# Performance work log

Hardware: AMD Instinct MI355X
Metric: run time of the kernel (lower is better)

## Reference

```python
import jax, jax.numpy as jnp
import numpy as np

NEG_SLOPE = 0.2

def _gat(x_src, x_dst, W_src, W_dst, a_src, a_dst, bias, src, dst, num_dst):
    # Bipartite PyG GATConv, heads=1, concat, add_self_loops=False.
    h_src = x_src @ W_src              # [N_src, H]
    h_dst = x_dst @ W_dst              # [N_dst, H]
    # Per-edge attention logits: leaky_relu(a_src.h_src[i] + a_dst.h_dst[j])
    e = jax.nn.leaky_relu((h_src @ a_src)[src] + (h_dst @ a_dst)[dst], NEG_SLOPE)  # [E]
    # Segment softmax over incoming edges of each dst node
    m = jax.ops.segment_max(e, dst, num_segments=num_dst)
    m = jnp.where(jnp.isfinite(m), m, 0.0)  # empty segments -> safe
    ex = jnp.exp(e - m[dst])
    denom = jax.ops.segment_sum(ex, dst, num_segments=num_dst)
    alpha = ex / denom[dst]            # [E]
    # Scatter-sum weighted source messages
    out = jax.ops.segment_sum(alpha[:, None] * h_src[src], dst, num_segments=num_dst)
    return out + bias


def setup_inputs() -> dict:
    key = jax.random.key(0)
    ks = jax.random.split(key, 20)
    N_L, N_A, D, H, O, E = 100000, 20000, 128, 128, 64, 500000
    s = 1.0 / np.sqrt(D)
    inp = {
        'x_label': jax.random.normal(ks[0], (N_L, D), jnp.float32),
        'x_attr': jax.random.normal(ks[1], (N_A, D), jnp.float32),
        'W_src_la': jax.random.normal(ks[2], (D, H), jnp.float32) * s,
        'W_dst_la': jax.random.normal(ks[3], (D, H), jnp.float32) * s,
        'a_src_la': jax.random.normal(ks[4], (H,), jnp.float32) * s,
        'a_dst_la': jax.random.normal(ks[5], (H,), jnp.float32) * s,
        'b_la': jax.random.normal(ks[6], (H,), jnp.float32) * 0.01,
        'W_src_al': jax.random.normal(ks[7], (D, H), jnp.float32) * s,
        'W_dst_al': jax.random.normal(ks[8], (D, H), jnp.float32) * s,
        'a_src_al': jax.random.normal(ks[9], (H,), jnp.float32) * s,
        'a_dst_al': jax.random.normal(ks[10], (H,), jnp.float32) * s,
        'b_al': jax.random.normal(ks[11], (H,), jnp.float32) * 0.01,
        'W_lin': jax.random.normal(ks[12], (H, O), jnp.float32) * s,
        'b_lin': jax.random.normal(ks[13], (O,), jnp.float32) * 0.01,
        'edge_src_la': jax.random.randint(ks[14], (E,), 0, N_L, jnp.int32),
        'edge_dst_la': jax.random.randint(ks[15], (E,), 0, N_A, jnp.int32),
        'edge_src_al': jax.random.randint(ks[16], (E,), 0, N_A, jnp.int32),
        'edge_dst_al': jax.random.randint(ks[17], (E,), 0, N_L, jnp.int32),
    }
    return inp


def reference(x_label, x_attr, W_src_la, W_dst_la, a_src_la, a_dst_la, b_la,
              W_src_al, W_dst_al, a_src_al, a_dst_al, b_al, W_lin, b_lin,
              edge_src_la, edge_dst_la, edge_src_al, edge_dst_al):
    N_L = x_label.shape[0]
    N_A = x_attr.shape[0]
    # label -> attribute GAT (output for 'attribute' nodes)
    h_attr = _gat(x_label, x_attr, W_src_la, W_dst_la, a_src_la, a_dst_la, b_la,
                  edge_src_la, edge_dst_la, N_A)
    # attribute -> label GAT (output for 'label' nodes)
    h_label = _gat(x_attr, x_label, W_src_al, W_dst_al, a_src_al, a_dst_al, b_al,
                   edge_src_al, edge_dst_al, N_L)
    h_attr = jax.nn.relu(h_attr)  # computed as in original (unused downstream)
    h_label = jax.nn.relu(h_label)
    out = h_label @ W_lin + b_lin
    return out
```

## Files before the change

### kernel.cpp

```cpp
#include <hip/hip_runtime.h>
#include <math.h>

#define NEG_SLOPE 0.2f

typedef __attribute__((ext_vector_type(8))) short bf16x8;
typedef __attribute__((ext_vector_type(4))) float f32x4;

__device__ __forceinline__ unsigned short f2bf(float f) {
    unsigned u = __float_as_uint(f);
    unsigned r = (u + 0x7FFFu + ((u >> 16) & 1u)) >> 16;
    return (unsigned short)r;
}

__device__ __forceinline__ void acc8(float* a, uint4 u, float x) {
    a[0] += x * __uint_as_float(u.x << 16);
    a[1] += x * __uint_as_float(u.x & 0xFFFF0000u);
    a[2] += x * __uint_as_float(u.y << 16);
    a[3] += x * __uint_as_float(u.y & 0xFFFF0000u);
    a[4] += x * __uint_as_float(u.z << 16);
    a[5] += x * __uint_as_float(u.z & 0xFFFF0000u);
    a[6] += x * __uint_as_float(u.w << 16);
    a[7] += x * __uint_as_float(u.w & 0xFFFF0000u);
}

__device__ __forceinline__ unsigned pack2(unsigned short lo, unsigned short hi) {
    return (unsigned)lo | ((unsigned)hi << 16);
}

__global__ __launch_bounds__(256) void k_pre(
    const int* __restrict__ dst, int* __restrict__ deg, int E, int nbDeg,
    const float* __restrict__ Wd, const float* __restrict__ ad,
    const float* __restrict__ Ws, const float* __restrict__ as_,
    float* __restrict__ wdst, float* __restrict__ wsrc,
    const float* __restrict__ Wlin, unsigned short* __restrict__ Wb) {
    int b = blockIdx.x, t = threadIdx.x;
    if (b < nbDeg) {
        int i = b * 256 + t;
        if (i < E) atomicAdd(&deg[dst[i]], 1);
    } else if (b == nbDeg) {
        const float* W = (t < 128) ? Wd : Ws;
        const float* a = (t < 128) ? ad : as_;
        int d = t & 127;
        float s = 0.f;
        #pragma unroll 8
        for (int h = 0; h < 128; ++h) s += W[d * 128 + h] * a[h];
        if (t < 128) wdst[d] = s; else wsrc[d] = s;
    } else {
        int idx = (b - nbDeg - 1) * 256 + t;
        int col = idx >> 7, k = idx & 127;
        Wb[idx] = f2bf(Wlin[k * 64 + col]);
    }
}

__device__ __forceinline__ void rowdot_role(const float* __restrict__ X,
                                            const float* __restrict__ v,
                                            float* __restrict__ out, int n,
                                            int vb, int t) {
    int gw = vb * 4 + (t >> 6);
    int lane = t & 63;
    int half = lane >> 5, li = lane & 31;
    int row = gw * 2 + half;
    if (row >= n) return;
    const float4* X4 = (const float4*)X;
    const float4* V4 = (const float4*)v;
    float4 x = X4[(size_t)row * 32 + li];
    float4 b = V4[li];
    float p = x.x * b.x + x.y * b.y + x.z * b.z + x.w * b.w;
    #pragma unroll
    for (int off = 16; off; off >>= 1) p += __shfl_xor(p, off);
    if (li == 0) out[row] = p;
}

__device__ __forceinline__ void hsrc_role(const float* __restrict__ X,
                                          const float* __restrict__ W,
                                          unsigned short* __restrict__ Hb,
                                          int nrows, int row0, int t,
                                          float* __restrict__ Xs ) {
    #pragma unroll
    for (int i = 0; i < 16; ++i) {
        int idx = t + i * 256;
        int r = idx >> 7;
        Xs[r * 128 + (idx & 127)] = (row0 + r < nrows) ? X[(size_t)row0 * 128 + idx] : 0.f;
    }
    __syncthreads();
    int cg = t & 31, rg = t >> 5;
    float acc[4][4];
    #pragma unroll
    for (int i = 0; i < 4; ++i)
        #pragma unroll
        for (int j = 0; j < 4; ++j) acc[i][j] = 0.f;
    const float4* W4 = (const float4*)W;
    #pragma unroll 4
    for (int d = 0; d < 128; ++d) {
        float4 wv = W4[d * 32 + cg];
        float x0 = Xs[(rg * 4 + 0) * 128 + d], x1 = Xs[(rg * 4 + 1) * 128 + d];
        float x2 = Xs[(rg * 4 + 2) * 128 + d], x3 = Xs[(rg * 4 + 3) * 128 + d];
        acc[0][0] += x0 * wv.x; acc[0][1] += x0 * wv.y; acc[0][2] += x0 * wv.z; acc[0][3] += x0 * wv.w;
        acc[1][0] += x1 * wv.x; acc[1][1] += x1 * wv.y; acc[1][2] += x1 * wv.z; acc[1][3] += x1 * wv.w;
        acc[2][0] += x2 * wv.x; acc[2][1] += x2 * wv.y; acc[2][2] += x2 * wv.z; acc[2][3] += x2 * wv.w;
        acc[3][0] += x3 * wv.x; acc[3][1] += x3 * wv.y; acc[3][2] += x3 * wv.z; acc[3][3] += x3 * wv.w;
    }
    #pragma unroll
    for (int i = 0; i < 4; ++i) {
        int gr = row0 + rg * 4 + i;
        if (gr < nrows) {
            ushort4 o;
            o.x = f2bf(acc[i][0]); o.y = f2bf(acc[i][1]);
            o.z = f2bf(acc[i][2]); o.w = f2bf(acc[i][3]);
            *(ushort4*)&Hb[(size_t)gr * 128 + cg * 4] = o;
        }
    }
}

__global__ __launch_bounds__(256) void k_mid(
    const int* __restrict__ deg, int* __restrict__ bsum, int nScan, int n,
    const float* __restrict__ xL, const float* __restrict__ wdst,
    float* __restrict__ sdst, int nRL, int NL,
    const float* __restrict__ xA, const float* __restrict__ wsrc,
    float* __restrict__ ssrc, int nRA, int NA,
    const float* __restrict__ Wsrc, unsigned short* __restrict__ Hb) {
    __shared__ float smemf[32 * 128];
    int b = blockIdx.x, t = threadIdx.x;
    if (b < nScan) {
        int* sd = (int*)smemf;
        int base = b * 1024 + t * 4;
        int s = 0;
        #pragma unroll
        for (int i = 0; i < 4; ++i) if (base + i < n) s += deg[base + i];
        sd[t] = s;
        __syncthreads();
        for (int off = 128; off; off >>= 1) {
            if (t < off) sd[t] += sd[t + off];
            __syncthreads();
        }
        if (t == 0) bsum[b] = sd[0];
    } else if (b < nScan + nRL) {
        rowdot_role(xL, wdst, sdst, NL, b - nScan, t);
    } else if (b < nScan + nRL + nRA) {
        rowdot_role(xA, wsrc, ssrc, NA, b - nScan - nRL, t);
    } else {
        hsrc_role(xA, Wsrc, Hb, NA, (b - nScan - nRL - nRA) * 32, t, smemf);
    }
}

__global__ __launch_bounds__(128) void k_scanB(int* __restrict__ bsum, int nb,
                                               int* __restrict__ rowptr, int n, int E) {
    __shared__ int ss[128];
    int t = threadIdx.x;
    if (nb <= 128) {
        int v = (t < nb) ? bsum[t] : 0;
        ss[t] = v;
        __syncthreads();
        for (int off = 1; off < 128; off <<= 1) {
            int u = (t >= off) ? ss[t - off] : 0;
            __syncthreads();
            ss[t] += u;
            __syncthreads();
        }
        if (t < nb) bsum[t] = ss[t] - v;
    } else if (t == 0) {
        int run = 0;
        for (int i = 0; i < nb; ++i) { int v = bsum[i]; bsum[i] = run; run += v; }
    }
    if (t == 0) rowptr[n] = E;
}

__global__ __launch_bounds__(256) void k_scanC(const int* __restrict__ deg,
                                               const int* __restrict__ bsum,
                                               int* __restrict__ rowptr, int n) {
    __shared__ int ss[256];
    int t = threadIdx.x;
    int base = blockIdx.x * 1024 + t * 4;
    int d[4]; int tsum = 0;
    #pragma unroll
    for (int i = 0; i < 4; ++i) { d[i] = (base + i < n) ? deg[base + i] : 0; tsum += d[i]; }
    ss[t] = tsum;
    __syncthreads();
    for (int off = 1; off < 256; off <<= 1) {
        int v = (t >= off) ? ss[t - off] : 0;
        __syncthreads();
        ss[t] += v;
        __syncthreads();
    }
    int excl = ss[t] - tsum + bsum[blockIdx.x];
    #pragma unroll
    for (int i = 0; i < 4; ++i) {
        if (base + i < n) rowptr[base + i] = excl;
        excl += d[i];
    }
}

__global__ void k_scatter(const int* __restrict__ src, const int* __restrict__ dst,
                          const float* __restrict__ ssrc, const float* __restrict__ sdst,
                          const int* __restrict__ rowptr, int* __restrict__ cursor,
                          int2* __restrict__ csr_pair, int E) {
    int i = blockIdx.x * blockDim.x + threadIdx.x;
    if (i >= E) return;
    int s = src[i], d = dst[i];
    float e = ssrc[s] + sdst[d];
    e = e > 0.f ? e : NEG_SLOPE * e;
    float ex = __expf(e);
    int pos = rowptr[d] + atomicAdd(&cursor[d], 1);
    csr_pair[pos] = make_int2(s, __float_as_int(ex));
}

__global__ __launch_bounds__(256) void k_gatout(
    const int* __restrict__ rowptr, const int2* __restrict__ csr_pair,
    const unsigned short* __restrict__ Hb, const float* __restrict__ b_al,
    const unsigned short* __restrict__ Wb, const float* __restrict__ b_lin,
    float* __restrict__ out, int n) {
    __shared__ unsigned short Gs[64 * 128];
    int t = threadIdx.x;
    int wave = t >> 6, lane = t & 63;
    int grp = lane >> 4, gl = lane & 15;
    const uint4* H16 = (const uint4*)Hb;
    int row0b = blockIdx.x * 64;
    const float4* B4 = (const float4*)b_al;
    float4 bA = B4[gl * 2], bB = B4[gl * 2 + 1];

    #pragma unroll
    for (int rr = 0; rr < 4; ++rr) {
        int rl = wave * 16 + rr * 4 + grp;
        int row = row0b + rl;
        uint4 gpack = make_uint4(0u, 0u, 0u, 0u);
        if (row < n) {
            int beg = rowptr[row], end = rowptr[row + 1];
            float a[8];
            #pragma unroll
            for (int k = 0; k < 8; ++k) a[k] = 0.f;
            float denom = 0.f;
            int j = beg;
            for (; j + 4 <= end; j += 4) {
                int2 p0 = csr_pair[j], p1 = csr_pair[j + 1];
                int2 p2 = csr_pair[j + 2], p3 = csr_pair[j + 3];
                float x0 = __int_as_float(p0.y), x1 = __int_as_float(p1.y);
                float x2 = __int_as_float(p2.y), x3 = __int_as_float(p3.y);
                uint4 u0 = H16[(size_t)p0.x * 16 + gl];
                uint4 u1 = H16[(size_t)p1.x * 16 + gl];
                uint4 u2 = H16[(size_t)p2.x * 16 + gl];
                uint4 u3 = H16[(size_t)p3.x * 16 + gl];
                denom += (x0 + x1) + (x2 + x3);
                acc8(a, u0, x0); acc8(a, u1, x1); acc8(a, u2, x2); acc8(a, u3, x3);
            }
            for (; j + 2 <= end; j += 2) {
                int2 p0 = csr_pair[j], p1 = csr_pair[j + 1];
                float x0 = __int_as_float(p0.y), x1 = __int_as_float(p1.y);
                uint4 u0 = H16[(size_t)p0.x * 16 + gl];
                uint4 u1 = H16[(size_t)p1.x * 16 + gl];
                denom += x0 + x1;
                acc8(a, u0, x0); acc8(a, u1, x1);
            }
            if (j < end) {
                int2 p0 = csr_pair[j];
                float x0 = __int_as_float(p0.y);
                uint4 u0 = H16[(size_t)p0.x * 16 + gl];
                denom += x0;
                acc8(a, u0, x0);
            }
            float inv = denom > 0.f ? 1.f / denom : 0.f;
            unsigned short g0 = f2bf(fmaxf(a[0] * inv + bA.x, 0.f));
            unsigned short g1 = f2bf(fmaxf(a[1] * inv + bA.y, 0.f));
            unsigned short g2 = f2bf(fmaxf(a[2] * inv + bA.z, 0.f));
            unsigned short g3 = f2bf(fmaxf(a[3] * inv + bA.w, 0.f));
            unsigned short g4 = f2bf(fmaxf(a[4] * inv + bB.x, 0.f));
            unsigned short g5 = f2bf(fmaxf(a[5] * inv + bB.y, 0.f));
            unsigned short g6 = f2bf(fmaxf(a[6] * inv + bB.z, 0.f));
            unsigned short g7 = f2bf(fmaxf(a[7] * inv + bB.w, 0.f));
            gpack = make_uint4(pack2(g0, g1), pack2(g2, g3), pack2(g4, g5), pack2(g6, g7));
        }
        int slot = gl ^ (rl & 15);
        *(uint4*)&Gs[rl * 128 + slot * 8] = gpack;
    }
    __syncthreads();

    int m = lane & 15, kq = lane >> 4;
    int rl = wave * 16 + m;
    f32x4 acc0 = {0.f, 0.f, 0.f, 0.f};
    f32x4 acc1 = {0.f, 0.f, 0.f, 0.f};
    f32x4 acc2 = {0.f, 0.f, 0.f, 0.f};
    f32x4 acc3 = {0.f, 0.f, 0.f, 0.f};
    const bf16x8* B0 = (const bf16x8*)(Wb + (size_t)(0 * 16 + m) * 128);
    const bf16x8* B1 = (const bf16x8*)(Wb + (size_t)(1 * 16 + m) * 128);
    const bf16x8* B2 = (const bf16x8*)(Wb + (size_t)(2 * 16 + m) * 128);
    const bf16x8* B3 = (const bf16x8*)(Wb + (size_t)(3 * 16 + m) * 128);
    #pragma unroll
    for (int s = 0; s < 4; ++s) {
        int ci = s * 4 + kq;
        int slot = ci ^ m;
        bf16x8 a = *(const bf16x8*)&Gs[rl * 128 + slot * 8];
        acc0 = __builtin_amdgcn_mfma_f32_16x16x32_bf16(a, B0[ci], acc0, 0, 0, 0);
        acc1 = __builtin_amdgcn_mfma_f32_16x16x32_bf16(a, B1[ci], acc1, 0, 0, 0);
        acc2 = __builtin_amdgcn_mfma_f32_16x16x32_bf16(a, B2[ci], acc2, 0, 0, 0);
        acc3 = __builtin_amdgcn_mfma_f32_16x16x32_bf16(a, B3[ci], acc3, 0, 0, 0);
    }
    float bl0 = b_lin[0 * 16 + m], bl1 = b_lin[1 * 16 + m];
    float bl2 = b_lin[2 * 16 + m], bl3 = b_lin[3 * 16 + m];
    int row0 = row0b + wave * 16;
    #pragma unroll
    for (int j = 0; j < 4; ++j) {
        int row = row0 + kq * 4 + j;
        if (row < n) {
            float* orow = out + (size_t)row * 64;
            orow[0 * 16 + m] = acc0[j] + bl0;
            orow[1 * 16 + m] = acc1[j] + bl1;
            orow[2 * 16 + m] = acc2[j] + bl2;
            orow[3 * 16 + m] = acc3[j] + bl3;
        }
    }
}

extern "C" void kernel_launch(void* const* d_in, const int* in_sizes, int n_in,
                              void* d_out, int out_size, void* d_ws, size_t ws_size,
                              hipStream_t stream) {
    const float* x_label  = (const float*)d_in[0];
    const float* x_attr   = (const float*)d_in[1];
    const float* W_src_al = (const float*)d_in[7];
    const float* W_dst_al = (const float*)d_in[8];
    const float* a_src_al = (const float*)d_in[9];
    const float* a_dst_al = (const float*)d_in[10];
    const float* b_al     = (const float*)d_in[11];
    const float* W_lin    = (const float*)d_in[12];
    const float* b_lin    = (const float*)d_in[13];
    const int* edge_src   = (const int*)d_in[16];
    const int* edge_dst   = (const int*)d_in[17];

    const int D = 128;
    const int N_L = in_sizes[0] / D;
    const int N_A = in_sizes[1] / D;
    const int E   = in_sizes[16];

    const int nbDeg = (E + 255) / 256;
    const int nScan = (N_L + 1023) / 1024;
    const int nRL   = (N_L + 7) / 8;
    const int nRA   = (N_A + 7) / 8;
    const int nH    = (N_A + 31) / 32;

    float* ws = (float*)d_ws;
    float* s_src = ws;
    float* s_dst = s_src + N_A;
    float* wdst  = s_dst + N_L;
    float* wsrc  = wdst + 128;
    int*   deg    = (int*)(wsrc + 128);
    int*   cursor = deg + N_L;
    int*   bsum   = cursor + N_L;
    int*   rowptr = bsum + 128;
    int2*  csr_pair = (int2*)(rowptr + N_L + 4);
    unsigned short* Hb = (unsigned short*)(csr_pair + E);
    unsigned short* Wb = Hb + (size_t)N_A * 128;

    float* out = (float*)d_out;

    hipMemsetAsync(deg, 0, (size_t)2 * N_L * sizeof(int), stream);

    k_pre<<<nbDeg + 1 + 32, 256, 0, stream>>>(edge_dst, deg, E, nbDeg,
                                              W_dst_al, a_dst_al, W_src_al, a_src_al,
                                              wdst, wsrc, W_lin, Wb);
    k_mid<<<nScan + nRL + nRA + nH, 256, 0, stream>>>(
        deg, bsum, nScan, N_L,
        x_label, wdst, s_dst, nRL, N_L,
        x_attr, wsrc, s_src, nRA, N_A,
        W_src_al, Hb);
    k_scanB<<<1, 128, 0, stream>>>(bsum, nScan, rowptr, N_L, E);
    k_scanC<<<nScan, 256, 0, stream>>>(deg, bsum, rowptr, N_L);
    k_scatter<<<nbDeg, 256, 0, stream>>>(edge_src, edge_dst, s_src, s_dst,
                                         rowptr, cursor, csr_pair, E);
    k_gatout<<<(N_L + 63) / 64, 256, 0, stream>>>(rowptr, csr_pair, Hb, b_al,
                                                  Wb, b_lin, out, N_L);
}
```

Measured before the change: 257.5 us.

## Fold prefix-scan into k_mid and batch more rows per rowdot wave

Replaces the three-pass scan (block sums in k_mid, k_scanB, k_scanC) with a single scan role inside k_mid. Each scan block recomputes its prefix offset by summing all preceding degrees with int4 loads, then does its local scan. This removes two kernel launches and the serial dependency between them. The rowdot role now handles 4 rows per half-wave, cutting block count for the dot products, and the block order is changed so the GEMM blocks launch first. The cost is redundant prefix reads, which grow with block index, and extra registers per thread.

```diff
diff --git a/kernel.cpp b/kernel.cpp
--- a/kernel.cpp
+++ b/kernel.cpp
@@ -56,19 +56,34 @@
                                             const float* __restrict__ v,
                                             float* __restrict__ out, int n,
                                             int vb, int t) {
-    int gw = vb * 4 + (t >> 6);
-    int lane = t & 63;
+    int wave = t >> 6, lane = t & 63;
     int half = lane >> 5, li = lane & 31;
-    int row = gw * 2 + half;
-    if (row >= n) return;
+    int row0 = (vb * 4 + wave) * 8 + half;
     const float4* X4 = (const float4*)X;
     const float4* V4 = (const float4*)v;
-    float4 x = X4[(size_t)row * 32 + li];
-    float4 b = V4[li];
-    float p = x.x * b.x + x.y * b.y + x.z * b.z + x.w * b.w;
-    #pragma unroll
-    for (int off = 16; off; off >>= 1) p += __shfl_xor(p, off);
-    if (li == 0) out[row] = p;
+    float4 bv = V4[li];
+    float p[4];
+    #pragma unroll
+    for (int k = 0; k < 4; ++k) {
+        int row = row0 + 2 * k;
+        p[k] = 0.f;
+        if (row < n) {
+            float4 x = X4[(size_t)row * 32 + li];
+            p[k] = x.x * bv.x + x.y * bv.y + x.z * bv.z + x.w * bv.w;
+        }
+    }
+    #pragma unroll
+    for (int off = 16; off; off >>= 1) {
+        #pragma unroll
+        for (int k = 0; k < 4; ++k) p[k] += __shfl_xor(p[k], off);
+    }
+    if (li == 0) {
+        #pragma unroll
+        for (int k = 0; k < 4; ++k) {
+            int row = row0 + 2 * k;
+            if (row < n) out[row] = p[k];
+        }
+    }
 }
 
 __device__ __forceinline__ void hsrc_role(const float* __restrict__ X,
@@ -112,81 +127,62 @@
     }
 }
 
+__device__ __forceinline__ void scan_role(const int* __restrict__ deg,
+                                          int* __restrict__ rowptr, int n, int E,
+                                          int vb, int t, int* __restrict__ sd) {
+    const int4* deg4 = (const int4*)deg;
+    int nq = vb * 256;
+    int s = 0;
+    for (int i = t; i < nq; i += 256) {
+        int4 v = deg4[i];
+        s += (v.x + v.y) + (v.z + v.w);
+    }
+    sd[t] = s;
+    __syncthreads();
+    for (int off = 128; off; off >>= 1) {
+        if (t < off) sd[t] += sd[t + off];
+        __syncthreads();
+    }
+    int offset = sd[0];
+    __syncthreads();
+    int base = vb * 1024 + t * 4;
+    int d[4]; int tsum = 0;
+    #pragma unroll
+    for (int i = 0; i < 4; ++i) { d[i] = (base + i < n) ? deg[base + i] : 0; tsum += d[i]; }
+    sd[t] = tsum;
+    __syncthreads();
+    for (int off = 1; off < 256; off <<= 1) {
+        int v = (t >= off) ? sd[t - off] : 0;
+        __syncthreads();
+        sd[t] += v;
+        __syncthreads();
+    }
+    int excl = sd[t] - tsum + offset;
+    #pragma unroll
+    for (int i = 0; i < 4; ++i) {
+        if (base + i < n) rowptr[base + i] = excl;
+        excl += d[i];
+    }
+    if (vb == 0 && t == 0) rowptr[n] = E;
+}
+
 __global__ __launch_bounds__(256) void k_mid(
-    const int* __restrict__ deg, int* __restrict__ bsum, int nScan, int n,
+    const int* __restrict__ deg, int* __restrict__ rowptr, int nScan, int n, int E,
     const float* __restrict__ xL, const float* __restrict__ wdst,
     float* __restrict__ sdst, int nRL, int NL,
     const float* __restrict__ xA, const float* __restrict__ wsrc,
     float* __restrict__ ssrc, int nRA, int NA,
-    const float* __restrict__ Wsrc, unsigned short* __restrict__ Hb) {
+    const float* __restrict__ Wsrc, unsigned short* __restrict__ Hb, int nH) {
     __shared__ float smemf[32 * 128];
     int b = blockIdx.x, t = threadIdx.x;
-    if (b < nScan) {
-        int* sd = (int*)smemf;
-        int base = b * 1024 + t * 4;
-        int s = 0;
-        #pragma unroll
-        for (int i = 0; i < 4; ++i) if (base + i < n) s += deg[base + i];
-        sd[t] = s;
-        __syncthreads();
-        for (int off = 128; off; off >>= 1) {
-            if (t < off) sd[t] += sd[t + off];
-            __syncthreads();
-        }
-        if (t == 0) bsum[b] = sd[0];
-    } else if (b < nScan + nRL) {
-        rowdot_role(xL, wdst, sdst, NL, b - nScan, t);
-    } else if (b < nScan + nRL + nRA) {
-        rowdot_role(xA, wsrc, ssrc, NA, b - nScan - nRL, t);
+    if (b < nH) {
+        hsrc_role(xA, Wsrc, Hb, NA, b * 32, t, smemf);
+    } else if (b < nH + nRL) {
+        rowdot_role(xL, wdst, sdst, NL, b - nH, t);
+    } else if (b < nH + nRL + nRA) {
+        rowdot_role(xA, wsrc, ssrc, NA, b - nH - nRL, t);
     } else {
-        hsrc_role(xA, Wsrc, Hb, NA, (b - nScan - nRL - nRA) * 32, t, smemf);
-    }
-}
-
-__global__ __launch_bounds__(128) void k_scanB(int* __restrict__ bsum, int nb,
-                                               int* __restrict__ rowptr, int n, int E) {
-    __shared__ int ss[128];
-    int t = threadIdx.x;
-    if (nb <= 128) {
-        int v = (t < nb) ? bsum[t] : 0;
-        ss[t] = v;
-        __syncthreads();
-        for (int off = 1; off < 128; off <<= 1) {
-            int u = (t >= off) ? ss[t - off] : 0;
-            __syncthreads();
-            ss[t] += u;
-            __syncthreads();
-        }
-        if (t < nb) bsum[t] = ss[t] - v;
-    } else if (t == 0) {
-        int run = 0;
-        for (int i = 0; i < nb; ++i) { int v = bsum[i]; bsum[i] = run; run += v; }
-    }
-    if (t == 0) rowptr[n] = E;
-}
-
-__global__ __launch_bounds__(256) void k_scanC(const int* __restrict__ deg,
-                                               const int* __restrict__ bsum,
-                                               int* __restrict__ rowptr, int n) {
-    __shared__ int ss[256];
-    int t = threadIdx.x;
-    int base = blockIdx.x * 1024 + t * 4;
-    int d[4]; int tsum = 0;
-    #pragma unroll
-    for (int i = 0; i < 4; ++i) { d[i] = (base + i < n) ? deg[base + i] : 0; tsum += d[i]; }
-    ss[t] = tsum;
-    __syncthreads();
-    for (int off = 1; off < 256; off <<= 1) {
-        int v = (t >= off) ? ss[t - off] : 0;
-        __syncthreads();
-        ss[t] += v;
-        __syncthreads();
-    }
-    int excl = ss[t] - tsum + bsum[blockIdx.x];
-    #pragma unroll
-    for (int i = 0; i < 4; ++i) {
-        if (base + i < n) rowptr[base + i] = excl;
-        excl += d[i];
+        scan_role(deg, rowptr, n, E, b - nH - nRL - nRA, t, (int*)smemf);
     }
 }
 
@@ -331,8 +327,8 @@
 
     const int nbDeg = (E + 255) / 256;
     const int nScan = (N_L + 1023) / 1024;
-    const int nRL   = (N_L + 7) / 8;
-    const int nRA   = (N_A + 7) / 8;
+    const int nRL   = (N_L + 31) / 32;
+    const int nRA   = (N_A + 31) / 32;
     const int nH    = (N_A + 31) / 32;
 
     float* ws = (float*)d_ws;
@@ -342,8 +338,7 @@
     float* wsrc  = wdst + 128;
     int*   deg    = (int*)(wsrc + 128);
     int*   cursor = deg + N_L;
-    int*   bsum   = cursor + N_L;
-    int*   rowptr = bsum + 128;
+    int*   rowptr = cursor + N_L;
     int2*  csr_pair = (int2*)(rowptr + N_L + 4);
     unsigned short* Hb = (unsigned short*)(csr_pair + E);
     unsigned short* Wb = Hb + (size_t)N_A * 128;
@@ -355,13 +350,11 @@
     k_pre<<<nbDeg + 1 + 32, 256, 0, stream>>>(edge_dst, deg, E, nbDeg,
                                               W_dst_al, a_dst_al, W_src_al, a_src_al,
                                               wdst, wsrc, W_lin, Wb);
-    k_mid<<<nScan + nRL + nRA + nH, 256, 0, stream>>>(
-        deg, bsum, nScan, N_L,
+    k_mid<<<nH + nRL + nRA + nScan, 256, 0, stream>>>(
+        deg, rowptr, nScan, N_L, E,
         x_label, wdst, s_dst, nRL, N_L,
         x_attr, wsrc, s_src, nRA, N_A,
-        W_src_al, Hb);
-    k_scanB<<<1, 128, 0, stream>>>(bsum, nScan, rowptr, N_L, E);
-    k_scanC<<<nScan, 256, 0, stream>>>(deg, bsum, rowptr, N_L);
+        W_src_al, Hb, nH);
     k_scatter<<<nbDeg, 256, 0, stream>>>(edge_src, edge_dst, s_src, s_dst,
                                          rowptr, cursor, csr_pair, E);
     k_gatout<<<(N_L + 63) / 64, 256, 0, stream>>>(rowptr, csr_pair, Hb, b_al,
```

Measured after the change: 242.1 us. 6.0% less time.
